# Performance work log

Measured on AMD Instinct MI355X. Metric: run time of the kernel, lower is better.

## Reference

```python
import jax, jax.numpy as jnp
import numpy as np

B, S, D, DH = 4, 2048, 1024, 64


def setup_inputs() -> dict:
    key = jax.random.key(0)
    ks = jax.random.split(key, 7)
    x = jax.random.normal(ks[0], (B, S, D), dtype=jnp.float32)
    def w(k):
        return jax.random.normal(k, (D, DH), dtype=jnp.float32) / np.sqrt(D).astype(np.float32)
    return {
        'x': x,
        'w_q_u': w(ks[1]), 'w_k_u': w(ks[2]), 'w_v_u': w(ks[3]),
        'w_q_c': w(ks[4]), 'w_k_c': w(ks[5]), 'w_v_c': w(ks[6]),
    }


def reference(x, w_q_u, w_k_u, w_v_u, w_q_c, w_k_c, w_v_c):
    b, n, _ = x.shape
    scale = w_q_u.shape[-1] ** -0.5
    # projections (LinearNoBias -> plain matmul)
    Q_u = x @ w_q_u
    K_u = x @ w_k_u
    V_u = x @ w_v_u
    Q_c = x @ w_q_c
    K_c = x @ w_k_c
    V_c = x @ w_v_c

    i = jnp.arange(n)
    causal = i[:, None] >= i[None, :]        # True where j <= i (binary causal / keep for S_c)
    lookahead = i[:, None] < i[None, :]      # True where j > i (allowed in sigmoid term)

    # term1: [b, n, n], zeroed above the diagonal via binary causal mask
    term1 = jnp.einsum('bid,bjd->bij', Q_c, V_u) * scale * causal.astype(x.dtype)

    # sigmoid gate: lookahead mask adds -inf on/below the diagonal -> sigmoid = 0 there
    logits_u = jnp.einsum('bid,bjd->bij', Q_u, K_u) * scale
    sigmoid_term = jax.nn.sigmoid(jnp.where(lookahead, logits_u, -jnp.inf))

    # nested n^3 matmul: S_u[b,i,k] = sum_j term1[b,i,j] * sigmoid_term[b,k,j]
    S_u = jnp.einsum('bij,bkj->bik', term1, sigmoid_term)

    S_c = jnp.where(causal, jnp.einsum('bid,bjd->bij', Q_c, K_c) * scale, -jnp.inf)

    attn = jax.nn.softmax(S_c - jax.nn.silu(S_u), axis=-1)
    return jnp.einsum('bij,bjd->bid', attn, V_c)
```

## Files before the change

### kernel.cpp

```cpp
#include <hip/hip_runtime.h>
#include <hip/hip_bf16.h>

typedef short bf16x8 __attribute__((ext_vector_type(8)));
typedef float f32x4  __attribute__((ext_vector_type(4)));
typedef _Float16 f16x8 __attribute__((ext_vector_type(8)));

#define MFMA16(a,b,c)  __builtin_amdgcn_mfma_f32_16x16x32_bf16((a),(b),(c),0,0,0)
#define MFMAF16(a,b,c) __builtin_amdgcn_mfma_f32_16x16x32_f16((a),(b),(c),0,0,0)

#define GLDS16(g,l) __builtin_amdgcn_global_load_lds( \
    (const __attribute__((address_space(1))) void*)(g), \
    (__attribute__((address_space(3))) void*)(l), 16, 0, 0)

struct P3Bins { unsigned char cnt[64]; unsigned char tiles[64][14]; };

__device__ __forceinline__ short f2bf(float f){
  union { float f; unsigned u; } v; v.f = f;
  unsigned r = v.u + 0x7fffu + ((v.u >> 16) & 1u);
  return (short)(r >> 16);
}
__device__ __forceinline__ float bf2f(short h){
  union { unsigned u; float f; } v; v.u = ((unsigned)(unsigned short)h) << 16;
  return v.f;
}
__device__ __forceinline__ void split8v(f32x4 a, f32x4 b, bf16x8& h, bf16x8& l){
  float t[8] = {a[0],a[1],a[2],a[3],b[0],b[1],b[2],b[3]};
  #pragma unroll
  for (int e = 0; e < 8; ++e){
    short hs = f2bf(t[e]);
    h[e] = hs;
    l[e] = f2bf(t[e] - bf2f(hs));
  }
}

__global__ void k_wt(const float* w0, const float* w1, const float* w2,
                     const float* w3, const float* w4, const float* w5,
                     unsigned short* __restrict__ wth, unsigned short* __restrict__ wtl){
  int p = blockIdx.y;
  const float* wp = p==0?w0:p==1?w1:p==2?w2:p==3?w3:p==4?w4:w5;
  int idx = blockIdx.x*256 + threadIdx.x;
  int n = idx >> 10, k = idx & 1023;
  float v = wp[k*64 + n];
  short hs = f2bf(v);
  wth[(size_t)p*65536 + n*1024 + k] = (unsigned short)hs;
  wtl[(size_t)p*65536 + n*1024 + k] = (unsigned short)f2bf(v - bf2f(hs));
}

__global__ void k_xsplit(const float* __restrict__ x,
                         unsigned short* __restrict__ xh, unsigned short* __restrict__ xl){
  size_t i = ((size_t)blockIdx.x*256 + threadIdx.x)*8;
  f32x4 a = *(const f32x4*)(x + i);
  f32x4 b = *(const f32x4*)(x + i + 4);
  bf16x8 h, l;
  split8v(a, b, h, l);
  *(bf16x8*)(xh + i) = h;
  *(bf16x8*)(xl + i) = l;
}

__global__ __launch_bounds__(256) void k_proj(
    const unsigned short* __restrict__ xh, const unsigned short* __restrict__ xl,
    const unsigned short* __restrict__ wth, const unsigned short* __restrict__ wtl,
    float* __restrict__ proj,
    unsigned short* __restrict__ projh, unsigned short* __restrict__ projl){
  __shared__ __align__(16) char sm[49152];
  int blk = blockIdx.x;
  int rb = blk/3, pg = blk - rb*3;
  int tid = threadIdx.x, w = tid >> 6, lane = tid & 63;
  int lm = lane & 15, quad = lane >> 4;
  int srow = lane >> 3, scg = (lane & 7) ^ srow;
  const char* xhg = (const char*)xh;
  const char* xlg = (const char*)xl;
  const char* w0h = (const char*)wth + (size_t)(pg*2  )*131072;
  const char* w0l = (const char*)wtl + (size_t)(pg*2  )*131072;
  const char* w1h = (const char*)wth + (size_t)(pg*2+1)*131072;
  const char* w1l = (const char*)wtl + (size_t)(pg*2+1)*131072;
  f32x4 acc[2][4] = {};
  for (int k0 = 0; k0 < 1024; k0 += 64){
    __syncthreads();
    size_t cb = (size_t)k0*2 + scg*16;
    #pragma unroll
    for (int i2 = 0; i2 < 2; ++i2){
      int i = w*2 + i2;
      size_t gx = (size_t)(rb*64 + i*8 + srow)*2048 + cb;
      size_t gw = (size_t)(i*8 + srow)*2048 + cb;
      GLDS16(xhg + gx, sm +         i*1024);
      GLDS16(xlg + gx, sm +  8192 + i*1024);
      GLDS16(w0h + gw, sm + 16384 + i*1024);
      GLDS16(w0l + gw, sm + 24576 + i*1024);
      GLDS16(w1h + gw, sm + 32768 + i*1024);
      GLDS16(w1l + gw, sm + 40960 + i*1024);
    }
    __syncthreads();
    #pragma unroll
    for (int ks = 0; ks < 2; ++ks){
      int ra = w*16 + lm;
      int offa = ra*128 + (((ks*4+quad) ^ (ra&7))*16);
      bf16x8 ah = *(const bf16x8*)(sm + offa);
      bf16x8 al = *(const bf16x8*)(sm + 8192 + offa);
      #pragma unroll
      for (int sub = 0; sub < 2; ++sub){
        #pragma unroll
        for (int n = 0; n < 4; ++n){
          int r = n*16 + lm;
          int off = r*128 + (((ks*4+quad) ^ (r&7))*16);
          bf16x8 bh = *(const bf16x8*)(sm + 16384 + sub*16384 + off);
          bf16x8 bl = *(const bf16x8*)(sm + 24576 + sub*16384 + off);
          acc[sub][n] = MFMA16(ah, bh, acc[sub][n]);
          acc[sub][n] = MFMA16(ah, bl, acc[sub][n]);
          acc[sub][n] = MFMA16(al, bh, acc[sub][n]);
        }
      }
    }
  }
  #pragma unroll
  for (int sub = 0; sub < 2; ++sub){
    int p = pg*2 + sub;
    if (p == 5){
      float* op = proj + (size_t)5*524288;
      #pragma unroll
      for (int n = 0; n < 4; ++n)
        #pragma unroll
        for (int e = 0; e < 4; ++e){
          int r = rb*64 + w*16 + quad*4 + e;
          op[(size_t)r*64 + n*16 + lm] = acc[sub][n][e];
        }
    } else {
      unsigned short* oph = projh + (size_t)p*524288;
      unsigned short* opl = projl + (size_t)p*524288;
      #pragma unroll
      for (int n = 0; n < 4; ++n)
        #pragma unroll
        for (int e = 0; e < 4; ++e){
          int r = rb*64 + w*16 + quad*4 + e;
          float f = acc[sub][n][e];
          short hs = f2bf(f);
          oph[(size_t)r*64 + n*16 + lm] = (unsigned short)hs;
          opl[(size_t)r*64 + n*16 + lm] = (unsigned short)f2bf(f - bf2f(hs));
        }
    }
  }
}

__global__ void k_vct(const float* __restrict__ proj, _Float16* __restrict__ vct){
  __shared__ float T[64][65];
  int b = blockIdx.y, st = blockIdx.x;
  int tid = threadIdx.x;
  const float* vc = proj + 5*524288 + (size_t)b*131072;
  int sloc = tid >> 2, cp = (tid & 3)*16;
  #pragma unroll
  for (int j = 0; j < 4; ++j){
    f32x4 v = *(const f32x4*)(vc + (size_t)(st*64 + sloc)*64 + cp + j*4);
    #pragma unroll
    for (int e = 0; e < 4; ++e) T[sloc][cp + j*4 + e] = v[e];
  }
  __syncthreads();
  int d = tid >> 2, sp = (tid & 3)*16;
  f16x8 h0, h1;
  #pragma unroll
  for (int j = 0; j < 8; ++j) h0[j] = (_Float16)T[sp + j][d];
  #pragma unroll
  for (int j = 0; j < 8; ++j) h1[j] = (_Float16)T[sp + 8 + j][d];
  size_t o = (size_t)b*131072 + (size_t)d*2048 + st*64 + sp;
  *(f16x8*)(vct + o) = h0; *(f16x8*)(vct + o + 8) = h1;
}

__global__ __launch_bounds__(256,2) void k_p2(
    const unsigned short* __restrict__ ph, const unsigned short* __restrict__ pl,
    _Float16* __restrict__ t1, _Float16* __restrict__ sg){
  __shared__ __align__(16) char sm[65536];
  int b = blockIdx.y;
  int t = blockIdx.x;
  bool isSig = t >= 136;
  if (isSig) t -= 136;
  int a = 0, bb = 0;
  #pragma unroll 1
  for (int aa = 0; aa < 16; ++aa){
    int c = isSig ? (16 - aa) : (aa + 1);
    if (t < c){ a = aa; bb = isSig ? (aa + t) : t; break; }
    t -= c;
  }
  int pa = isSig ? 0 : 3;
  int pb = isSig ? 1 : 2;
  const char* Ahg = (const char*)ph + (size_t)pa*1048576;
  const char* Alg = (const char*)pl + (size_t)pa*1048576;
  const char* Bhg = (const char*)ph + (size_t)pb*1048576;
  const char* Blg = (const char*)pl + (size_t)pb*1048576;
  int tid = threadIdx.x, w = tid >> 6, lane = tid & 63;
  int lm = lane & 15, quad = lane >> 4;
  int srow = lane >> 3, scg = (lane & 7) ^ srow;
  int wm = (w & 1)*64, wn = (w >> 1)*64;
  #pragma unroll
  for (int i2 = 0; i2 < 4; ++i2){
    int i = w*4 + i2;
    int rl = i*8 + srow;
    size_t ga = (size_t)(b*2048 + a*128  + rl)*128 + scg*16;
    size_t gb = (size_t)(b*2048 + bb*128 + rl)*128 + scg*16;
    GLDS16(Ahg + ga, sm +         i*1024);
    GLDS16(Alg + ga, sm + 16384 + i*1024);
    GLDS16(Bhg + gb, sm + 32768 + i*1024);
    GLDS16(Blg + gb, sm + 49152 + i*1024);
  }
  __syncthreads();
  f32x4 acc[4][4] = {};
  #pragma unroll
  for (int ks = 0; ks < 2; ++ks){
    bf16x8 bh[4], bl[4];
    #pragma unroll
    for (int n = 0; n < 4; ++n){
      int r = wn + n*16 + lm;
      int off = r*128 + (((ks*4+quad) ^ (r&7))*16);
      bh[n] = *(const bf16x8*)(sm + 32768 + off);
      bl[n] = *(const bf16x8*)(sm + 49152 + off);
    }
    #pragma unroll
    for (int m = 0; m < 4; ++m){
      int r = wm + m*16 + lm;
      int off = r*128 + (((ks*4+quad) ^ (r&7))*16);
      bf16x8 ah = *(const bf16x8*)(sm + off);
      bf16x8 al = *(const bf16x8*)(sm + 16384 + off);
      #pragma unroll
      for (int n = 0; n < 4; ++n){
        acc[m][n] = MFMA16(ah, bh[n], acc[m][n]);
        acc[m][n] = MFMA16(ah, bl[n], acc[m][n]);
        acc[m][n] = MFMA16(al, bh[n], acc[m][n]);
      }
    }
  }
  __syncthreads();
  _Float16* Tt = (_Float16*)sm;
  #pragma unroll
  for (int m = 0; m < 4; ++m){
    #pragma unroll
    for (int n = 0; n < 4; ++n){
      #pragma unroll
      for (int e = 0; e < 4; ++e){
        int il = wm + m*16 + quad*4 + e;
        int jl = wn + n*16 + lm;
        int gi = a*128 + il, gj = bb*128 + jl;
        float v = acc[m][n][e] * 0.125f;
        float outv;
        if (!isSig) outv = (gj <= gi) ? v : 0.0f;
        else        outv = (gj >  gi) ? (1.0f/(1.0f + __expf(-v))) : 0.0f;
        Tt[il*128 + jl] = (_Float16)outv;
      }
    }
  }
  __syncthreads();
  _Float16* outp = (isSig ? sg : t1) + (size_t)b*4194304;
  #pragma unroll
  for (int r = 0; r < 8; ++r){
    int lrow = w*32 + r*4 + (lane >> 4);
    int c16 = lane & 15;
    f32x4 vv = *(const f32x4*)(sm + lrow*256 + c16*16);
    *(f32x4*)((char*)(outp + (size_t)(a*128 + lrow)*2048 + bb*128) + c16*16) = vv;
  }
}

__global__ __launch_bounds__(256,2) void k_p3(
    const unsigned short* __restrict__ ph, const unsigned short* __restrict__ pl,
    const _Float16* __restrict__ t1, const _Float16* __restrict__ sg,
    _Float16* __restrict__ lg, P3Bins bz){
  __shared__ __align__(16) char sm[65536];
  int bin = blockIdx.x;
  int b = blockIdx.y;
  int tid = threadIdx.x, w = tid >> 6, lane = tid & 63;
  int lm = lane & 15, quad = lane >> 4;
  size_t mat = (size_t)b * 4194304;
  const char* Ag = (const char*)(t1 + mat);
  const char* Bg = (const char*)(sg + mat);
  int srow = lane >> 3, scg = (lane & 7) ^ srow;
  int wm = (w & 1)*64, wn = (w >> 1)*64;
  int ntiles = bz.cnt[bin];

  for (int tix = 0; tix < ntiles; ++tix){
    int tv = bz.tiles[bin][tix];
    int I = tv >> 4, K = tv & 15;
    int nsteps = 2*(I - K) + 2;
    int j0 = 2*K;
    __syncthreads();

    auto stage = [&](int j64, int base){
      size_t colb = (size_t)j64*128 + scg*16;
      #pragma unroll
      for (int i2 = 0; i2 < 4; ++i2){
        int i = w*4 + i2;
        int rl = i*8 + srow;
        GLDS16(Ag + (size_t)(I*128 + rl)*4096 + colb, sm + base +         i*1024);
        GLDS16(Bg + (size_t)(K*128 + rl)*4096 + colb, sm + base + 16384 + i*1024);
      }
    };

    f32x4 su[4][4] = {};
    stage(j0, 0);
    for (int step = 0; step < nsteps; ++step){
      int cur = (step & 1) << 15;
      __syncthreads();
      if (step + 1 < nsteps) stage(j0 + step + 1, (~step & 1) << 15);
      #pragma unroll
      for (int ks = 0; ks < 2; ++ks){
        f16x8 bf[4];
        #pragma unroll
        for (int n = 0; n < 4; ++n){
          int r = wn + n*16 + lm;
          bf[n] = *(const f16x8*)(sm + cur + 16384 + r*128 + (((ks*4+quad) ^ (r&7))*16));
        }
        #pragma unroll
        for (int m = 0; m < 4; ++m){
          int r = wm + m*16 + lm;
          f16x8 af = *(const f16x8*)(sm + cur + r*128 + (((ks*4+quad) ^ (r&7))*16));
          #pragma unroll
          for (int n = 0; n < 4; ++n)
            su[m][n] = MFMAF16(af, bf[n], su[m][n]);
        }
      }
    }
    const char* Qh = (const char*)ph + (size_t)3*1048576;
    const char* Ql = (const char*)pl + (size_t)3*1048576;
    const char* Kh = (const char*)ph + (size_t)4*1048576;
    const char* Kl = (const char*)pl + (size_t)4*1048576;
    f32x4 sc[4][4] = {};
    #pragma unroll
    for (int ks = 0; ks < 2; ++ks){
      bf16x8 kh[4], kl[4];
      #pragma unroll
      for (int n = 0; n < 4; ++n){
        size_t off = (size_t)(b*2048 + K*128 + wn + n*16 + lm)*128 + (ks*32 + quad*8)*2;
        kh[n] = *(const bf16x8*)(Kh + off);
        kl[n] = *(const bf16x8*)(Kl + off);
      }
      #pragma unroll
      for (int m = 0; m < 4; ++m){
        size_t off = (size_t)(b*2048 + I*128 + wm + m*16 + lm)*128 + (ks*32 + quad*8)*2;
        bf16x8 ah = *(const bf16x8*)(Qh + off);
        bf16x8 al = *(const bf16x8*)(Ql + off);
        #pragma unroll
        for (int n = 0; n < 4; ++n){
          sc[m][n] = MFMA16(ah, kh[n], sc[m][n]);
          sc[m][n] = MFMA16(ah, kl[n], sc[m][n]);
          sc[m][n] = MFMA16(al, kh[n], sc[m][n]);
        }
      }
    }
    __syncthreads();
    _Float16* Tt = (_Float16*)sm;
    #pragma unroll
    for (int m = 0; m < 4; ++m){
      #pragma unroll
      for (int n = 0; n < 4; ++n){
        #pragma unroll
        for (int e = 0; e < 4; ++e){
          int il = wm + m*16 + quad*4 + e;
          int jl = wn + n*16 + lm;
          float xv = su[m][n][e];
          float sgm = 1.0f/(1.0f + __expf(-xv));
          Tt[il*128 + jl] = (_Float16)(sc[m][n][e]*0.125f - xv*sgm);
        }
      }
    }
    __syncthreads();
    _Float16* lgb = lg + mat;
    #pragma unroll
    for (int r = 0; r < 8; ++r){
      int lrow = w*32 + r*4 + (lane >> 4);
      int c16 = lane & 15;
      f32x4 vv = *(const f32x4*)(sm + lrow*256 + c16*16);
      *(f32x4*)((char*)(lgb + (size_t)(I*128 + lrow)*2048 + K*128) + c16*16) = vv;
    }
  }
}

__global__ __launch_bounds__(256,2) void k_p4(const _Float16* __restrict__ lg,
    const _Float16* __restrict__ vct, float* __restrict__ out){
  __shared__ __align__(16) char sm[66048];
  float* Mz = (float*)(sm + 65536);
  float* Sz = (float*)(sm + 65792);
  int b = blockIdx.y;
  int b1 = blockIdx.x;
  int tid = threadIdx.x, w = tid >> 6, lane = tid & 63;
  int lm = lane & 15, quad = lane >> 4;
  const _Float16* vb = vct + (size_t)b*131072;
  for (int pass = 0; pass < 2; ++pass){
    int band = pass ? (127 - b1) : b1;
    int r0 = band*16;
    const char* lgb = (const char*)lg + ((size_t)b*4194304 + (size_t)r0*2048)*2;
    int nkt = ((r0 + 15) >> 6) + 1;
    int fc = (r0 + 1) >> 6;
    int srl = lane >> 3, ssl = lane & 7;
    __syncthreads();
    for (int kt = w; kt < nkt; kt += 4){
      #pragma unroll
      for (int i2 = 0; i2 < 2; ++i2){
        int rl = i2*8 + srl;
        GLDS16(lgb + (size_t)rl*4096 + kt*128 + ((ssl ^ (rl & 7))*16),
               sm + kt*2048 + i2*1024);
      }
    }
    __syncthreads();
    float m_r = -3.0e38f;
    for (int kt = w; kt < nkt; kt += 4){
      #pragma unroll
      for (int half = 0; half < 2; ++half){
        int sl = quad*2 + half;
        f16x8 v = *(const f16x8*)(sm + kt*2048 + lm*128 + ((sl ^ (lm & 7))*16));
        int cb = kt*64 + sl*8;
        #pragma unroll
        for (int e = 0; e < 8; ++e)
          m_r = (cb + e <= r0 + lm) ? fmaxf(m_r, (float)v[e]) : m_r;
      }
    }
    m_r = fmaxf(m_r, __shfl_xor(m_r, 16));
    m_r = fmaxf(m_r, __shfl_xor(m_r, 32));
    Mz[w*16 + lm] = m_r;
    __syncthreads();
    float mfin = fmaxf(fmaxf(Mz[lm], Mz[16 + lm]), fmaxf(Mz[32 + lm], Mz[48 + lm]));
    float s_r = 0.0f;
    for (int kt = w; kt < nkt; kt += 4){
      #pragma unroll
      for (int half = 0; half < 2; ++half){
        int sl = quad*2 + half;
        f16x8 v = *(const f16x8*)(sm + kt*2048 + lm*128 + ((sl ^ (lm & 7))*16));
        int cb = kt*64 + sl*8;
        #pragma unroll
        for (int e = 0; e < 8; ++e)
          if (cb + e <= r0 + lm) s_r += __expf((float)v[e] - mfin);
      }
    }
    s_r += __shfl_xor(s_r, 16);
    s_r += __shfl_xor(s_r, 32);
    Sz[w*16 + lm] = s_r;
    f32x4 acc[4] = {};
    for (int kt = w; kt < nkt; kt += 4){
      bool full = kt < fc;
      #pragma unroll
      for (int ks = 0; ks < 2; ++ks){
        f16x8 Lv = *(const f16x8*)(sm + kt*2048 + lm*128 + (((ks*4+quad) ^ (lm & 7))*16));
        int jbase = kt*64 + ks*32 + quad*8;
        f16x8 af;
        #pragma unroll
        for (int e = 0; e < 8; ++e){
          float p = __expf((float)Lv[e] - mfin);
          if (!full && (jbase + e > r0 + lm)) p = 0.0f;
          af[e] = (_Float16)p;
        }
        #pragma unroll
        for (int n = 0; n < 4; ++n){
          f16x8 bv = *(const f16x8*)(vb + (size_t)(n*16 + lm)*2048 + jbase);
          acc[n] = MFMAF16(af, bv, acc[n]);
        }
      }
    }
    __syncthreads();
    float* Ot = (float*)sm;
    #pragma unroll
    for (int n = 0; n < 4; ++n)
      #pragma unroll
      for (int e = 0; e < 4; ++e)
        Ot[(w*16 + quad*4 + e)*64 + n*16 + lm] = acc[n][e];
    __syncthreads();
    int row = tid >> 4, c4 = (tid & 15)*4;
    f32x4 s = *(const f32x4*)&Ot[row*64 + c4];
    #pragma unroll
    for (int ww = 1; ww < 4; ++ww){
      f32x4 t2 = *(const f32x4*)&Ot[(ww*16 + row)*64 + c4];
      s[0]+=t2[0]; s[1]+=t2[1]; s[2]+=t2[2]; s[3]+=t2[3];
    }
    float z = Sz[row] + Sz[16 + row] + Sz[32 + row] + Sz[48 + row];
    f32x4 o = { s[0]/z, s[1]/z, s[2]/z, s[3]/z };
    *(f32x4*)(out + ((size_t)b*2048 + r0 + row)*64 + c4) = o;
  }
}

static const size_t OFF_PROJ  = 0;
static const size_t OFF_WTH   = 12582912;
static const size_t OFF_WTL   = 13369344;
static const size_t OFF_PROJH = 14155776;
static const size_t OFF_PROJL = 20447232;
static const size_t OFF_VCT   = 26738688;
static const size_t OFF_T1    = 27787264;
static const size_t OFF_SG    = 61341696;
static const size_t OFF_LG    = 94896128;
static const size_t OFF_XH    = 128450560;
static const size_t OFF_XL    = 145227776;

static P3Bins build_bins(){
  P3Bins bz;
  int load[64];
  for (int i = 0; i < 64; ++i){ bz.cnt[i] = 0; load[i] = 0; }
  for (int d = 15; d >= 0; --d){
    for (int K = 0; K + d < 16; ++K){
      int I = K + d;
      int len = 2*d + 2;
      int best = 0;
      for (int bin = 1; bin < 64; ++bin) if (load[bin] < load[best]) best = bin;
      load[best] += len;
      bz.tiles[best][bz.cnt[best]++] = (unsigned char)(I*16 + K);
    }
  }
  return bz;
}

extern "C" void kernel_launch(void* const* d_in, const int* in_sizes, int n_in,
                              void* d_out, int out_size, void* d_ws, size_t ws_size,
                              hipStream_t stream){
  (void)in_sizes; (void)n_in; (void)out_size; (void)ws_size;
  const float* x = (const float*)d_in[0];
  char* ws = (char*)d_ws;
  float*          proj  = (float*)(ws + OFF_PROJ);
  unsigned short* wth   = (unsigned short*)(ws + OFF_WTH);
  unsigned short* wtl   = (unsigned short*)(ws + OFF_WTL);
  unsigned short* projh = (unsigned short*)(ws + OFF_PROJH);
  unsigned short* projl = (unsigned short*)(ws + OFF_PROJL);
  _Float16*       vct   = (_Float16*)(ws + OFF_VCT);
  _Float16*       t1    = (_Float16*)(ws + OFF_T1);
  _Float16*       sg    = (_Float16*)(ws + OFF_SG);
  _Float16*       lg    = (_Float16*)(ws + OFF_LG);
  unsigned short* xh    = (unsigned short*)(ws + OFF_XH);
  unsigned short* xl    = (unsigned short*)(ws + OFF_XL);

  P3Bins bz = build_bins();

  k_wt    <<<dim3(256,6),  256, 0, stream>>>((const float*)d_in[1], (const float*)d_in[2],
                                             (const float*)d_in[3], (const float*)d_in[4],
                                             (const float*)d_in[5], (const float*)d_in[6], wth, wtl);
  k_xsplit<<<dim3(4096),   256, 0, stream>>>(x, xh, xl);
  k_proj  <<<dim3(384),    256, 0, stream>>>(xh, xl, wth, wtl, proj, projh, projl);
  k_vct   <<<dim3(32,4),   256, 0, stream>>>(proj, vct);
  k_p2    <<<dim3(272,4),  256, 0, stream>>>(projh, projl, t1, sg);
  k_p3    <<<dim3(64,4),   256, 0, stream>>>(projh, projl, t1, sg, lg, bz);
  k_p4    <<<dim3(64,4),   256, 0, stream>>>(lg, vct, (float*)d_out);
}
```

Before: 213.3 us.

## Store x, weights and t1/sigmoid in 64-column panels; double p3 bins

The split x and weight buffers are rewritten in a K-panel-major layout of 64-element column chunks, so each staging step in the projection kernel reads one contiguous 128-byte row segment per row. The t1 and sigmoid matrices get the same panel-major layout, which makes the nested n^3 kernel's tile loads contiguous within a panel instead of strided across 4 KB rows. Separately, the p3 load-balancing bins grow from 64 to 128 per batch and the grid doubles, to use more CUs with shorter per-block tile lists. This risks more blocks with uneven finish times, and every producer and consumer of these buffers must agree on the new layout.

```diff
diff --git a/kernel.cpp b/kernel.cpp
--- a/kernel.cpp
+++ b/kernel.cpp
@@ -12,7 +12,7 @@
     (const __attribute__((address_space(1))) void*)(g), \
     (__attribute__((address_space(3))) void*)(l), 16, 0, 0)
 
-struct P3Bins { unsigned char cnt[64]; unsigned char tiles[64][14]; };
+struct P3Bins { unsigned char cnt[128]; unsigned char tiles[128][4]; };
 
 __device__ __forceinline__ short f2bf(float f){
   union { float f; unsigned u; } v; v.f = f;
@@ -42,19 +42,22 @@
   int n = idx >> 10, k = idx & 1023;
   float v = wp[k*64 + n];
   short hs = f2bf(v);
-  wth[(size_t)p*65536 + n*1024 + k] = (unsigned short)hs;
-  wtl[(size_t)p*65536 + n*1024 + k] = (unsigned short)f2bf(v - bf2f(hs));
+  size_t d = (size_t)p*65536 + (size_t)(k>>6)*4096 + n*64 + (k&63);
+  wth[d] = (unsigned short)hs;
+  wtl[d] = (unsigned short)f2bf(v - bf2f(hs));
 }
 
 __global__ void k_xsplit(const float* __restrict__ x,
                          unsigned short* __restrict__ xh, unsigned short* __restrict__ xl){
   size_t i = ((size_t)blockIdx.x*256 + threadIdx.x)*8;
+  int s = (int)(i >> 10), k = (int)(i & 1023);
   f32x4 a = *(const f32x4*)(x + i);
   f32x4 b = *(const f32x4*)(x + i + 4);
   bf16x8 h, l;
   split8v(a, b, h, l);
-  *(bf16x8*)(xh + i) = h;
-  *(bf16x8*)(xl + i) = l;
+  size_t d = (size_t)(k>>6)*524288 + (size_t)s*64 + (k&63);
+  *(bf16x8*)(xh + d) = h;
+  *(bf16x8*)(xl + d) = l;
 }
 
 __global__ __launch_bounds__(256) void k_proj(
@@ -76,13 +79,14 @@
   const char* w1l = (const char*)wtl + (size_t)(pg*2+1)*131072;
   f32x4 acc[2][4] = {};
   for (int k0 = 0; k0 < 1024; k0 += 64){
-    __syncthreads();
-    size_t cb = (size_t)k0*2 + scg*16;
+    int kp = k0 >> 6;
+    __syncthreads();
     #pragma unroll
     for (int i2 = 0; i2 < 2; ++i2){
       int i = w*2 + i2;
-      size_t gx = (size_t)(rb*64 + i*8 + srow)*2048 + cb;
-      size_t gw = (size_t)(i*8 + srow)*2048 + cb;
+      int rl = i*8 + srow;
+      size_t gx = (size_t)kp*1048576 + (size_t)(rb*64 + rl)*128 + scg*16;
+      size_t gw = (size_t)kp*8192 + (size_t)rl*128 + scg*16;
       GLDS16(xhg + gx, sm +         i*1024);
       GLDS16(xlg + gx, sm +  8192 + i*1024);
       GLDS16(w0h + gw, sm + 16384 + i*1024);
@@ -246,13 +250,15 @@
     }
   }
   __syncthreads();
-  _Float16* outp = (isSig ? sg : t1) + (size_t)b*4194304;
+  char* outp = (char*)(isSig ? sg : t1);
   #pragma unroll
   for (int r = 0; r < 8; ++r){
     int lrow = w*32 + r*4 + (lane >> 4);
     int c16 = lane & 15;
+    int jp = 2*bb + (c16 >> 3);
     f32x4 vv = *(const f32x4*)(sm + lrow*256 + c16*16);
-    *(f32x4*)((char*)(outp + (size_t)(a*128 + lrow)*2048 + bb*128) + c16*16) = vv;
+    size_t d = ((size_t)(b*32 + jp)*2048 + a*128 + lrow)*128 + (c16 & 7)*16;
+    *(f32x4*)(outp + d) = vv;
   }
 }
 
@@ -265,9 +271,8 @@
   int b = blockIdx.y;
   int tid = threadIdx.x, w = tid >> 6, lane = tid & 63;
   int lm = lane & 15, quad = lane >> 4;
-  size_t mat = (size_t)b * 4194304;
-  const char* Ag = (const char*)(t1 + mat);
-  const char* Bg = (const char*)(sg + mat);
+  const char* Ag = (const char*)t1;
+  const char* Bg = (const char*)sg;
   int srow = lane >> 3, scg = (lane & 7) ^ srow;
   int wm = (w & 1)*64, wn = (w >> 1)*64;
   int ntiles = bz.cnt[bin];
@@ -280,13 +285,13 @@
     __syncthreads();
 
     auto stage = [&](int j64, int base){
-      size_t colb = (size_t)j64*128 + scg*16;
+      size_t pbase = (size_t)(b*32 + j64)*2048;
       #pragma unroll
       for (int i2 = 0; i2 < 4; ++i2){
         int i = w*4 + i2;
         int rl = i*8 + srow;
-        GLDS16(Ag + (size_t)(I*128 + rl)*4096 + colb, sm + base +         i*1024);
-        GLDS16(Bg + (size_t)(K*128 + rl)*4096 + colb, sm + base + 16384 + i*1024);
+        GLDS16(Ag + (pbase + I*128 + rl)*128 + scg*16, sm + base +         i*1024);
+        GLDS16(Bg + (pbase + K*128 + rl)*128 + scg*16, sm + base + 16384 + i*1024);
       }
     };
 
@@ -358,7 +363,7 @@
       }
     }
     __syncthreads();
-    _Float16* lgb = lg + mat;
+    _Float16* lgb = lg + (size_t)b*4194304;
     #pragma unroll
     for (int r = 0; r < 8; ++r){
       int lrow = w*32 + r*4 + (lane >> 4);
@@ -484,14 +489,14 @@
 
 static P3Bins build_bins(){
   P3Bins bz;
-  int load[64];
-  for (int i = 0; i < 64; ++i){ bz.cnt[i] = 0; load[i] = 0; }
+  int load[128];
+  for (int i = 0; i < 128; ++i){ bz.cnt[i] = 0; load[i] = 0; }
   for (int d = 15; d >= 0; --d){
     for (int K = 0; K + d < 16; ++K){
       int I = K + d;
       int len = 2*d + 2;
       int best = 0;
-      for (int bin = 1; bin < 64; ++bin) if (load[bin] < load[best]) best = bin;
+      for (int bin = 1; bin < 128; ++bin) if (load[bin] < load[best]) best = bin;
       load[best] += len;
       bz.tiles[best][bz.cnt[best]++] = (unsigned char)(I*16 + K);
     }
@@ -526,6 +531,6 @@
   k_proj  <<<dim3(384),    256, 0, stream>>>(xh, xl, wth, wtl, proj, projh, projl);
   k_vct   <<<dim3(32,4),   256, 0, stream>>>(proj, vct);
   k_p2    <<<dim3(272,4),  256, 0, stream>>>(projh, projl, t1, sg);
-  k_p3    <<<dim3(64,4),   256, 0, stream>>>(projh, projl, t1, sg, lg, bz);
+  k_p3    <<<dim3(128,4),  256, 0, stream>>>(projh, projl, t1, sg, lg, bz);
   k_p4    <<<dim3(64,4),   256, 0, stream>>>(lg, vct, (float*)d_out);
 }
```

After: 214.0 us. Within noise of the previous version (+0.3%).
